# Optimization experiments

Measured on AMD Instinct MI355X. Metric: run time of the kernel, lower is better.

Reference implementation:

```python
import jax, jax.numpy as jnp
import numpy as np

# ---- para constants (see shape_source) ----
SIZE = 200          # SLM / detector plane
PAD = 100           # para.paddings -> padded FFT plane 400x400
PADDED = SIZE + 2 * PAD
NUM_LAYERS = 4
SCALE = 2.0         # para.scale
EXT = 1.0           # para.extension
K = 8               # para.kernel_size
S = 8               # para.stride
M = (SIZE - K) // S + 1   # para.map_size = 25
WIN = 5             # para.win_size
T = 1.0             # softmax temperature
RANGE = 10          # para.range (== dim_out)
DIM_OUT = 10
HIDDEN = 512
DIM_IN = M * M      # 625, flattened BN output feeds fcl
THR = 0.2           # para.thershold
SHIFT = 0.0         # para.shift
EPS = 1e-5          # BatchNorm eps
BATCH = 32


def setup_inputs() -> dict:
    key = jax.random.key(0)
    ks = jax.random.split(key, 10)
    x = jax.random.uniform(ks[0], (BATCH, SIZE, SIZE), jnp.float32)

    def transfer(k):  # unit-magnitude angular-spectrum transfer function
        ph = jax.random.uniform(k, (PADDED, PADDED), jnp.float32, 0.0, 2.0 * np.pi)
        return jnp.exp(1j * ph).astype(jnp.complex64)

    h = transfer(ks[1])
    h_pro = transfer(ks[2])
    h_det = transfer(ks[3])
    phase = 0.1 * jax.random.normal(ks[4], (NUM_LAYERS, SIZE, SIZE), jnp.float32)
    W1 = 0.02 * jax.random.normal(ks[5], (HIDDEN, DIM_IN), jnp.float32)
    b1 = jnp.zeros((HIDDEN,), jnp.float32)
    W2 = 0.02 * jax.random.normal(ks[6], (DIM_OUT, HIDDEN), jnp.float32)
    b2 = jnp.zeros((DIM_OUT,), jnp.float32)
    gamma = jnp.ones((1,), jnp.float32)   # BatchNorm2d(1) weight
    beta = jnp.zeros((1,), jnp.float32)   # BatchNorm2d(1) bias
    return {"x": x, "batch_size": BATCH, "h": h, "h_pro": h_pro, "h_det": h_det,
            "phase": phase, "W1": W1, "b1": b1, "W2": W2, "b2": b2,
            "gamma": gamma, "beta": beta}


def _diff(wave, trans):
    # F.pad + fftshift/fft2 * trans / ifft2/ifftshift (batch-dim shifts cancel)
    wave = jnp.pad(wave, ((0, 0), (PAD, PAD), (PAD, PAD)))
    wf = jnp.fft.fft2(jnp.fft.fftshift(wave, axes=(-2, -1)))
    return jnp.fft.ifftshift(jnp.fft.ifft2(wf * trans), axes=(-2, -1))


def _forward(x, batch_size, h, h_pro, h_det, phase, W1, b1, W2, b2, gamma, beta):
    x = x.astype(jnp.complex64)
    x = _diff(x, h_pro)[:, PAD:PAD + SIZE, PAD:PAD + SIZE]
    for idx in range(NUM_LAYERS):
        trans = jnp.pad(phase[idx], ((PAD, PAD), (PAD, PAD)))
        w = _diff(x, h)
        w = w * jnp.exp(1j * SCALE * jnp.pi * (jnp.sin(EXT * trans) + 1.0))
        x = w[:, PAD:PAD + SIZE, PAD:PAD + SIZE]
    x = _diff(x, h_det)[:, PAD:PAD + SIZE, PAD:PAD + SIZE]
    i_out = jnp.square(jnp.abs(x))                       # (B, SIZE, SIZE)
    B = i_out.shape[0]
    # AvgPool2d(K, S) with SIZE % K == 0 -> reshape-mean
    pooled = i_out.reshape(B, M, K, M, K).mean(axis=(2, 4))  # (B, M, M)

    rows = jnp.arange(M)

    def window(i, j):
        rm = (rows >= i) & (rows < i + WIN)
        cm = (rows >= j) & (rows < j + WIN)
        mask = (rm[:, None] & cm[None, :]).astype(pooled.dtype)   # I_block
        sig = pooled * mask                                       # (B, M, M)
        # BatchNorm2d(1), training mode: stats over all N*H*W
        mu = sig.mean()
        var = sig.var()
        nrm = (sig - mu) / jnp.sqrt(var + EPS) * gamma[0] + beta[0]
        f = nrm.reshape(B, -1)                                    # (B, DIM_IN)
        hid = jax.nn.relu(f @ W1.T + b1)                          # dropout: eval
        logits = (hid @ W2.T + b2) / T
        p = jax.nn.softmax(logits, axis=1)                        # (B, DIM_OUT)
        a = jnp.argmax(p, axis=1)                                 # (B,)
        delta = p.max(axis=1) - p.min(axis=1)                     # b - b2
        temp = jax.nn.one_hot(a, RANGE + 1, dtype=jnp.float32).sum(0)
        final0 = jnp.argmax(temp)
        dm = delta * (a == final0).astype(delta.dtype)            # delta * delta_max
        nz = jnp.sum(dm != 0.0)                                   # csr .data length
        delta1 = jnp.where(nz > 0, dm.sum() / jnp.maximum(nz, 1).astype(dm.dtype), jnp.nan)
        # nan < THR is False, matching torch semantics
        final = jnp.where(delta1 < THR, 0, final0 + 1).astype(jnp.int32)
        res = jnp.where(final == 0, 0.0, final.astype(jnp.float32) + SHIFT)
        ch = (final != 0).astype(jnp.float32)
        return final, res, ch

    ii, jj = jnp.meshgrid(jnp.arange(M), jnp.arange(M), indexing="ij")
    finals, result, ch_map = jax.vmap(window)(ii.ravel(), jj.ravel())
    result = result.reshape(M, M)
    ch_map = ch_map.reshape(M, M)
    histo = jnp.zeros(RANGE + 1, jnp.float32).at[finals].add(1.0)
    return result, ch_map, histo


def reference(x, batch_size, h, h_pro, h_det, phase, W1, b1, W2, b2, gamma, beta):
    return _forward(x, batch_size, h, h_pro, h_det, phase, W1, b1, W2, b2, gamma, beta)
```

## Files before the change

kernel.cpp:

```cpp
#include <hip/hip_runtime.h>
#include <math.h>

#define GLIM_X    1280000
#define GLIM_H    160000
#define GLIM_PH   160000
#define GLIM_W1   320000
#define GLIM_B1   512
#define GLIM_W2   5120
#define GLIM_B2   10
#define GLIM_OUT  1261
#define GLIM_POOL 20000

#define HPART 128

struct cplx { float x, y; };
__device__ __forceinline__ cplx operator+(cplx a, cplx b){ return {a.x+b.x, a.y+b.y}; }
__device__ __forceinline__ cplx operator-(cplx a, cplx b){ return {a.x-b.x, a.y-b.y}; }
__device__ __forceinline__ cplx cmul(cplx a, cplx b){ return {a.x*b.x - a.y*b.y, a.x*b.y + a.y*b.x}; }
template<bool INV>
__device__ __forceinline__ cplx tw(cplx a, cplx w){
  if(INV) return {a.x*w.x + a.y*w.y, a.y*w.x - a.x*w.y};
  else    return {a.x*w.x - a.y*w.y, a.x*w.y + a.y*w.x};
}
template<bool INV>
__device__ __forceinline__ void dft4(cplx&a, cplx&b, cplx&c, cplx&d){
  cplx t0=a+c, t1=a-c, t2=b+d, t3=b-d;
  cplx j3 = INV ? cplx{-t3.y, t3.x} : cplx{t3.y, -t3.x};
  a = t0+t2; c = t0-t2; b = t1+j3; d = t1-j3;
}
template<bool INV>
__device__ void fft16(cplx* x, const cplx* tab){
  cplx y[16];
  #pragma unroll
  for(int b=0;b<4;b++){
    cplx p0=x[b], p1=x[4+b], p2=x[8+b], p3=x[12+b];
    dft4<INV>(p0,p1,p2,p3);
    y[b*4+0]=p0;
    y[b*4+1]=tw<INV>(p1, tab[25*b]);
    y[b*4+2]=tw<INV>(p2, tab[50*b]);
    y[b*4+3]=tw<INV>(p3, tab[75*b]);
  }
  #pragma unroll
  for(int c=0;c<4;c++){
    cplx p0=y[c], p1=y[4+c], p2=y[8+c], p3=y[12+c];
    dft4<INV>(p0,p1,p2,p3);
    x[c]=p0; x[c+4]=p1; x[c+8]=p2; x[c+12]=p3;
  }
}
template<bool INV>
__device__ __forceinline__ void dft5(const cplx* v, cplx* o, const cplx* tab){
  #pragma unroll
  for(int k=0;k<5;k++){
    cplx s=v[0];
    #pragma unroll
    for(int j=1;j<5;j++){
      const int m=(j*k)%5;
      s = s + tw<INV>(v[j], tab[80*m]);
    }
    o[k]=s;
  }
}
template<bool INV>
__device__ void fft25(cplx* t, const cplx* tab){
  cplx u[25];
  #pragma unroll
  for(int b=0;b<5;b++){
    cplx v[5], o[5];
    #pragma unroll
    for(int a=0;a<5;a++) v[a]=t[5*a+b];
    dft5<INV>(v,o,tab);
    #pragma unroll
    for(int c=0;c<5;c++) u[b*5+c]=tw<INV>(o[c], tab[16*b*c]);
  }
  #pragma unroll
  for(int c=0;c<5;c++){
    cplx v[5], o[5];
    #pragma unroll
    for(int b=0;b<5;b++) v[b]=u[b*5+c];
    dft5<INV>(v,o,tab);
    #pragma unroll
    for(int d=0;d<5;d++) t[c+5*d]=o[d];
  }
}

__device__ __forceinline__ float bf2f(unsigned short u){
  unsigned int v = ((unsigned int)u)<<16;
  float f; __builtin_memcpy(&f,&v,4); return f;
}
__device__ __forceinline__ float hf2f(unsigned short u){
  _Float16 x; __builtin_memcpy(&x,&u,2); return (float)x;
}
__device__ __forceinline__ cplx ldH(const void* p, int i, int dec){
  if(i<0 || i>=GLIM_H) return {0.f,0.f};
  unsigned int v = ((const unsigned int*)p)[i];
  unsigned short lo=(unsigned short)(v&0xFFFFu), hi=(unsigned short)(v>>16);
  cplx z;
  if(dec==2)      z = { hf2f(lo), hf2f(hi) };
  else if(dec==3) z = { (float)(short)lo*(1.f/32767.f), (float)(short)hi*(1.f/32767.f) };
  else            z = { bf2f(lo), bf2f(hi) };
  if(!(fabsf(z.x) < 2.f)) z.x = 0.f;
  if(!(fabsf(z.y) < 2.f)) z.y = 0.f;
  return z;
}
__device__ __forceinline__ float ldf(const float* p, int i, int lim){
  if(i<0 || i>=lim) return 0.f;
  return p[i];
}
__device__ __forceinline__ void stout(float* p, int i, float v){
  if(i>=0 && i<GLIM_OUT) p[i] = v;
}

__global__ __launch_bounds__(64) void k_probe(const void* h, int* flags){
  __shared__ float err[3];
  if(threadIdx.x<3) err[threadIdx.x]=0.f;
  __syncthreads();
  if(threadIdx.x<32){
    unsigned int v = ((const unsigned int*)h)[threadIdx.x];
    unsigned short lo=(unsigned short)(v&0xFFFFu), hi=(unsigned short)(v>>16);
    float cr[3], ci[3];
    cr[0]=bf2f(lo);                       ci[0]=bf2f(hi);
    cr[1]=hf2f(lo);                       ci[1]=hf2f(hi);
    cr[2]=(float)(short)lo*(1.f/32767.f); ci[2]=(float)(short)hi*(1.f/32767.f);
    for(int d=0;d<3;d++){
      float r2 = cr[d]*cr[d] + ci[d]*ci[d];
      float e = fabsf(r2 - 1.f);
      if(!(e < 4.f)) e = 4.f;
      atomicAdd(&err[d], e);
    }
  }
  __syncthreads();
  if(threadIdx.x==0){
    int best=0; float be=err[0];
    for(int d=1; d<3; d++) if(err[d] < be){ be=err[d]; best=d; }
    flags[1] = best+1;
    flags[0] = 0;
  }
}

__global__ __launch_bounds__(256) void k_init(cplx* tab, float* outz, float* hist, float* pr){
  int t = blockIdx.x*256 + threadIdx.x;
  if(t < 400){
    float a = -6.28318530717958647692f * (float)t * (1.0f/400.0f);
    float sn, cs; sincosf(a, &sn, &cs);
    tab[t] = { cs, sn };
  }
  if(t < GLIM_OUT) outz[t] = 0.f;
  if(t < 11) hist[t] = 0.f;
  if(t >= 16 && t < 30) pr[t-16] = 0.f;
}

__global__ __launch_bounds__(256) void k_hprep(const void* h, const void* hpro,
    const void* hdet, cplx* __restrict__ Hd, const int* __restrict__ flags)
{
  int dec = flags[1];
  int t = blockIdx.x*256 + threadIdx.x;
  if(t >= 3*GLIM_H) return;
  int arr = t/GLIM_H, o = t - arr*GLIM_H;
  int c = o/400, rem = o - c*400;
  int k1 = rem/25, k2 = rem - k1*25;
  const void* src = (arr==0)?h:((arr==1)?hpro:hdet);
  Hd[t] = ldH(src, (k1+16*k2)*400 + c, dec);
}

__global__ __launch_bounds__(256,2) void k_rowfft(const float* __restrict__ xr,
    int img0, cplx* __restrict__ A, const cplx* __restrict__ gtab, int alim, int nimg)
{
  __shared__ cplx lt[8*400];
  __shared__ cplx stab[400];
  for(int m=threadIdx.x;m<400;m+=256) stab[m]=gtab[m];
  int lr = threadIdx.x>>5, role = threadIdx.x&31;
  int img_local = blockIdx.x % nimg;
  int rc = (blockIdx.x / nimg)*8 + lr;
  int abase = img_local*80000 + rc*400;
  __syncthreads();
  if(role<25){
    int n2=role;
    cplx x[16];
    #pragma unroll
    for(int n1=0;n1<16;n1++){
      cplx v={0.f,0.f};
      if(n1>=4 && n1<12){
        int cc = 25*n1+n2-100;
        v = { ldf(xr, (img0+img_local)*40000 + rc*200 + cc, GLIM_X), 0.f };
      }
      x[n1]=v;
    }
    fft16<false>(x, stab);
    cplx* L = lt + lr*400;
    #pragma unroll
    for(int k1=0;k1<16;k1++) L[k1*25+n2]=tw<false>(x[k1], stab[n2*k1]);
  }
  __syncthreads();
  if(role<16){
    int k1=role;
    cplx* L = lt + lr*400;
    cplx t[25];
    #pragma unroll
    for(int n2=0;n2<25;n2++) t[n2]=L[k1*25+n2];
    fft25<false>(t, stab);
    #pragma unroll
    for(int k2=0;k2<25;k2++){
      int ai = abase + k1+16*k2;
      if(ai>=0 && ai<alim) A[ai]=t[k2];
    }
  }
}

__global__ __launch_bounds__(512,2) void k_colpass(cplx* __restrict__ A,
    const cplx* __restrict__ Hd, const cplx* __restrict__ gtab, int nimg)
{
  __shared__ cplx lt[16*401];
  __shared__ cplx stab[400];
  for(int m=threadIdx.x;m<400;m+=512) stab[m]=gtab[m];
  int img_local = blockIdx.x % nimg, cg = blockIdx.x / nimg;
  int col0 = cg*16;
  int lc = threadIdx.x&15, rr = threadIdx.x>>4;
  int abase = img_local*80000 + col0 + lc;
  cplx* L = lt + lc*401;
  cplx xx[25];
  __syncthreads();
  if(rr<25){
    int n2=rr;
    #pragma unroll
    for(int n1=0;n1<16;n1++){
      cplx v={0.f,0.f};
      if(n1>=4 && n1<12) v = A[abase + (25*n1+n2-100)*400];
      xx[n1]=v;
    }
    fft16<false>(xx, stab);
    #pragma unroll
    for(int k1=0;k1<16;k1++) L[k1*25+n2]=tw<false>(xx[k1], stab[n2*k1]);
  }
  __syncthreads();
  if(rr<16){
    int k1=rr;
    #pragma unroll
    for(int n2=0;n2<25;n2++) xx[n2]=L[k1*25+n2];
    fft25<false>(xx, stab);
    const cplx* hrun = Hd + (col0+lc)*400 + k1*25;
    #pragma unroll
    for(int k2=0;k2<25;k2++) L[k1*25+k2]=cmul(xx[k2], hrun[k2]);
  }
  __syncthreads();
  if(rr<25){
    int n2=rr;
    #pragma unroll
    for(int n1=0;n1<16;n1++){
      int m = 25*n1+n2;
      xx[n1] = L[(m&15)*25 + (m>>4)];
    }
  }
  __syncthreads();
  if(rr<25){
    int n2=rr;
    fft16<true>(xx, stab);
    #pragma unroll
    for(int k1=0;k1<16;k1++) L[k1*25+n2]=tw<true>(xx[k1], stab[n2*k1]);
  }
  __syncthreads();
  if(rr<16){
    int k1=rr;
    #pragma unroll
    for(int n2=0;n2<25;n2++) xx[n2]=L[k1*25+n2];
    fft25<true>(xx, stab);
    const float sc=1.0f/400.0f;
    #pragma unroll
    for(int k2=0;k2<25;k2++){
      int m=k1+16*k2;
      if(m>=100 && m<300) A[abase + (m-100)*400] = { xx[k2].x*sc, xx[k2].y*sc };
    }
  }
}

__global__ __launch_bounds__(512,2) void k_rowpass(cplx* __restrict__ A,
    const float* __restrict__ ph, int phoff, int useMask,
    const cplx* __restrict__ gtab, int alim, int nimg)
{
  __shared__ cplx lt[16*401];
  __shared__ cplx stab[400];
  for(int m=threadIdx.x;m<400;m+=512) stab[m]=gtab[m];
  int lc = threadIdx.x&15, rr = threadIdx.x>>4;
  int img_local = blockIdx.x % nimg, rg = blockIdx.x / nimg;
  int rc = rg*16 + lc;
  int valid = rc < 200;
  int abase = img_local*80000 + rc*400;
  cplx* L = lt + lc*401;
  cplx xx[25];
  __syncthreads();
  if(rr<25){
    int n2=rr;
    #pragma unroll
    for(int n1=0;n1<16;n1++){
      cplx v={0.f,0.f};
      int ai = abase + 25*n1+n2;
      if(valid && ai>=0 && ai<alim) v=A[ai];
      xx[n1]=v;
    }
    fft16<true>(xx, stab);
    #pragma unroll
    for(int k1=0;k1<16;k1++) L[k1*25+n2]=tw<true>(xx[k1], stab[n2*k1]);
  }
  __syncthreads();
  if(rr<16){
    int k1=rr;
    #pragma unroll
    for(int n2=0;n2<25;n2++) xx[n2]=L[k1*25+n2];
    fft25<true>(xx, stab);
    const float sc=1.0f/400.0f;
    #pragma unroll
    for(int k2=0;k2<25;k2++){
      int m=k1+16*k2;
      if(m>=100 && m<300){
        int cc=m-100;
        cplx v={ xx[k2].x*sc, xx[k2].y*sc };
        if(useMask){
          float tt = ldf(ph, phoff + rc*200+cc, GLIM_PH);
          float th = 6.28318530717958647692f*(sinf(tt)+1.0f);
          float sn, cs; sincosf(th,&sn,&cs);
          v = cmul(v, cplx{cs,sn});
        }
        xx[k2]=v;
      }
    }
  }
  __syncthreads();
  if(rr<16){
    int k1=rr;
    #pragma unroll
    for(int k2=0;k2<25;k2++){
      int m=k1+16*k2;
      if(m>=100 && m<300) L[m-100]=xx[k2];
    }
  }
  __syncthreads();
  if(rr<25){
    int n2=rr;
    #pragma unroll
    for(int n1=0;n1<16;n1++){
      cplx v={0.f,0.f};
      if(n1>=4 && n1<12) v = L[25*n1+n2-100];
      xx[n1]=v;
    }
    fft16<false>(xx, stab);
    #pragma unroll
    for(int k1=0;k1<16;k1++) L[k1*25+n2]=tw<false>(xx[k1], stab[n2*k1]);
  }
  __syncthreads();
  if(rr<16){
    int k1=rr;
    #pragma unroll
    for(int n2=0;n2<25;n2++) xx[n2]=L[k1*25+n2];
    fft25<false>(xx, stab);
    if(valid){
      #pragma unroll
      for(int k2=0;k2<25;k2++){
        int ai = abase + k1+16*k2;
        if(ai>=0 && ai<alim) A[ai]=xx[k2];
      }
    }
  }
}

__global__ __launch_bounds__(256,2) void k_rowpool(const cplx* __restrict__ A,
    float* __restrict__ pooled, int img0, const cplx* __restrict__ gtab, int alim, int nimg)
{
  __shared__ cplx lt[8*400];
  __shared__ cplx stab[400];
  __shared__ float sI[8][200];
  for(int m=threadIdx.x;m<400;m+=256) stab[m]=gtab[m];
  int lr=threadIdx.x>>5, role=threadIdx.x&31;
  int img_local = blockIdx.x % nimg, rg = blockIdx.x / nimg;
  int abase = img_local*80000 + (rg*8+lr)*400;
  __syncthreads();
  if(role<25){
    int n2=role;
    cplx x[16];
    #pragma unroll
    for(int n1=0;n1<16;n1++){
      cplx v={0.f,0.f};
      int ai = abase + 25*n1+n2;
      if(ai>=0 && ai<alim) v=A[ai];
      x[n1]=v;
    }
    fft16<true>(x, stab);
    cplx* L = lt + lr*400;
    #pragma unroll
    for(int k1=0;k1<16;k1++) L[k1*25+n2]=tw<true>(x[k1], stab[n2*k1]);
  }
  __syncthreads();
  cplx t[25];
  int k1 = role;
  if(role<16){
    cplx* L=lt+lr*400;
    #pragma unroll
    for(int n2=0;n2<25;n2++) t[n2]=L[k1*25+n2];
    fft25<true>(t, stab);
    const float sc=1.0f/400.0f;
    #pragma unroll
    for(int k2=0;k2<25;k2++){ t[k2].x*=sc; t[k2].y*=sc; }
  }
  if(role<16){
    #pragma unroll
    for(int k2=0;k2<25;k2++){
      int m=k1+16*k2;
      if(m>=100 && m<300) sI[lr][m-100] = t[k2].x*t[k2].x + t[k2].y*t[k2].y;
    }
  }
  __syncthreads();
  if(threadIdx.x<25){
    int il = img_local, r0 = rg*8;
    float s=0.f;
    #pragma unroll
    for(int u=0;u<8;u++){
      #pragma unroll
      for(int v=0;v<8;v++) s += sI[u][threadIdx.x*8+v];
    }
    int pi = (img0+il)*625 + (r0>>3)*25 + threadIdx.x;
    if(pi>=0 && pi<GLIM_POOL) pooled[pi] = s*(1.0f/64.0f);
  }
}

__global__ __launch_bounds__(64) void k_rowsum(const float* __restrict__ W1,
    float* __restrict__ rs){
  __shared__ float red[64];
  int hh = blockIdx.x;
  float s=0.f;
  for(int e=threadIdx.x;e<625;e+=64) s += ldf(W1, hh*625+e, GLIM_W1);
  red[threadIdx.x]=s;
  __syncthreads();
  for(int off=32;off>0;off>>=1){
    if(threadIdx.x<off) red[threadIdx.x]+=red[threadIdx.x+off];
    __syncthreads();
  }
  if(threadIdx.x==0 && hh<512) rs[hh]=red[0];
}

__global__ __launch_bounds__(256,2) void k_window(const float* __restrict__ pooled,
    const float* __restrict__ W1, const float* __restrict__ b1,
    const float* __restrict__ W2, const float* __restrict__ rowsum,
    const float* __restrict__ gm, const float* __restrict__ bt,
    float* __restrict__ LP)
{
  __shared__ float w1s[HPART*26];
  __shared__ float w2s[10*HPART];
  __shared__ float ps[25*32];
  __shared__ float comb[HPART];
  __shared__ int   wIdx[25];
  __shared__ float sred[4][2];
  __shared__ float sf0, sgos;

  int wi = blockIdx.x >> 2;
  int part = blockIdx.x & 3;
  int h0 = part*HPART;
  int i = wi/25, j = wi - i*25;
  int er = (25-i<5)?(25-i):5;
  int ec = (25-j<5)?(25-j):5;
  int E = er*ec;
  int tid = threadIdx.x;
  if(tid<25) wIdx[tid] = (i + tid/ec)*25 + (j + tid%ec);
  __syncthreads();

  for(int t=tid;t<10*HPART;t+=256) w2s[t] = ldf(W2, (t>>7)*512 + h0 + (t&(HPART-1)), GLIM_W2);

  for(int t=tid;t<800;t+=256){
    int e=t>>5;
    float v=0.f;
    if(e<E){
      v = pooled[(t&31)*625 + wIdx[e]];
      if(!(fabsf(v) < 1e30f)) v = 0.f;
    }
    ps[t]=v;
  }

  if(E==25){
    for(int t=tid;t<HPART*25;t+=256){
      int hh=t/25, e=t-hh*25;
      w1s[hh*26+e] = ldf(W1, (h0+hh)*625+wIdx[e], GLIM_W1);
    }
  } else {
    for(int t=tid;t<832;t+=256) ((float4*)w1s)[t] = float4{0.f,0.f,0.f,0.f};
    __syncthreads();
    for(int t=tid;t<HPART*E;t+=256){
      int hh=t/E, e=t-hh*E;
      w1s[hh*26+e] = ldf(W1, (h0+hh)*625+wIdx[e], GLIM_W1);
    }
  }
  __syncthreads();

  {
    float s1=0.f, s2=0.f;
    for(int t=tid;t<800;t+=256){ float v=ps[t]; s1+=v; s2+=v*v; }
    #pragma unroll
    for(int m=1;m<64;m<<=1){ s1 += __shfl_xor(s1,m); s2 += __shfl_xor(s2,m); }
    if((tid&63)==0){ sred[tid>>6][0]=s1; sred[tid>>6][1]=s2; }
  }
  __syncthreads();
  if(tid==0){
    float a=sred[0][0]+sred[1][0]+sred[2][0]+sred[3][0];
    float c=sred[0][1]+sred[1][1]+sred[2][1]+sred[3][1];
    float mu = a*(1.0f/20000.0f);
    float var = c*(1.0f/20000.0f) - mu*mu;
    float sg = sqrtf(var + 1e-5f);
    float g = gm[0];
    sf0 = bt[0] - g*mu/sg;
    sgos = g/sg;
  }
  __syncthreads();
  float f0=sf0, gos=sgos;
  for(int hh=tid;hh<HPART;hh+=256) comb[hh] = ldf(b1,h0+hh,GLIM_B1) + f0*ldf(rowsum,h0+hh,512);
  __syncthreads();

  int b = tid&31, s = tid>>5;
  float psr[25];
  #pragma unroll
  for(int e=0;e<25;e++) psr[e]=ps[e*32+b];

  float pl[10];
  #pragma unroll
  for(int o=0;o<10;o++) pl[o]=0.f;
  for(int k=0;k<16;k++){
    int hh = s*16+k;
    const float* wr = &w1s[hh*26];
    float wsum=0.f;
    #pragma unroll
    for(int e=0;e<25;e++) wsum = fmaf(wr[e], psr[e], wsum);
    float acc = comb[hh] + gos*wsum;
    float hid = acc>0.f?acc:0.f;
    #pragma unroll
    for(int o=0;o<10;o++) pl[o] = fmaf(hid, w2s[o*HPART+hh], pl[o]);
  }
  __syncthreads();
  float* red = w1s;
  #pragma unroll
  for(int o=0;o<10;o++) red[(s*32+b)*10+o]=pl[o];
  __syncthreads();

  if(tid<32){
    #pragma unroll
    for(int o=0;o<10;o++){
      float a = 0.f;
      #pragma unroll
      for(int u=0;u<8;u++) a += red[(u*32+tid)*10+o];
      LP[((part*625+wi)*32+tid)*10+o] = a;
    }
  }
}

__global__ __launch_bounds__(64) void k_vote(const float* __restrict__ LP,
    const float* __restrict__ b2, float* __restrict__ outp, float* __restrict__ hist)
{
  __shared__ int aArr[32];
  __shared__ float dArr[32];
  int wi = blockIdx.x, tid = threadIdx.x;
  if(tid<32){
    float lg[10];
    #pragma unroll
    for(int o=0;o<10;o++){
      float a = ldf(b2,o,GLIM_B2);
      #pragma unroll
      for(int p=0;p<4;p++) a += LP[((p*625+wi)*32+tid)*10+o];
      lg[o]=a;
    }
    float lmax=lg[0]; int am=0;
    #pragma unroll
    for(int o=1;o<10;o++) if(lg[o]>lmax){lmax=lg[o]; am=o;}
    float lmin=lg[0];
    #pragma unroll
    for(int o=1;o<10;o++) lmin=fminf(lmin,lg[o]);
    float Z=0.f;
    #pragma unroll
    for(int o=0;o<10;o++) Z += expf(lg[o]-lmax);
    float delta = (1.f - expf(lmin-lmax))/Z;
    aArr[tid]=am; dArr[tid]=delta;
  }
  __syncthreads();
  if(tid==0){
    int votes[11];
    #pragma unroll
    for(int k=0;k<11;k++) votes[k]=0;
    for(int bb=0;bb<32;bb++){
      int a=aArr[bb];
      if(a>=0 && a<11) votes[a]++;
    }
    int f0i=0, bv=votes[0];
    #pragma unroll
    for(int k=1;k<11;k++) if(votes[k]>bv){bv=votes[k]; f0i=k;}
    float sum=0.f; int nz=0;
    for(int bb=0;bb<32;bb++){
      if(aArr[bb]==f0i){
        float dd=dArr[bb];
        sum+=dd;
        if(dd!=0.f) nz++;
      }
    }
    int fin;
    if(nz>0){
      float d1=sum/(float)nz;
      fin = (d1<0.2f)?0:(f0i+1);
    } else fin = f0i+1;
    stout(outp, wi, (fin==0)?0.f:(float)fin);
    stout(outp, 625+wi, (fin!=0)?1.f:0.f);
    if(fin>=0 && fin<=10) atomicAdd(&hist[fin], 1.0f);
  }
}

__global__ __launch_bounds__(64) void k_fin(const float* __restrict__ hist,
    float* __restrict__ outp){
  if(threadIdx.x<11) stout(outp, 1250+threadIdx.x, hist[threadIdx.x]);
}

__global__ __launch_bounds__(256) void k_diag(const float* __restrict__ pooled,
    const float* __restrict__ hist, const float* __restrict__ pr,
    const int* __restrict__ flags, float* __restrict__ outp){
  __shared__ float smax[256];
  __shared__ int snan[256];
  float m=0.f; int nan=0;
  for(int i=threadIdx.x;i<GLIM_POOL;i+=256){
    float v=pooled[i];
    if(isnan(v)||isinf(v)) nan=1;
    else { float a=fabsf(v); if(a>m)m=a; }
  }
  smax[threadIdx.x]=m; snan[threadIdx.x]=nan;
  __syncthreads();
  for(int off=128;off>0;off>>=1){
    if(threadIdx.x<off){
      smax[threadIdx.x]=fmaxf(smax[threadIdx.x],smax[threadIdx.x+off]);
      snan[threadIdx.x]|=snan[threadIdx.x+off];
    }
    __syncthreads();
  }
  if(threadIdx.x==0 && hist[0] < 613.f){
    int dec = flags[1] & 7;
    int low, nanbit = 0;
    if(snan[0]){ nanbit=128; low=0; (void)pr; }
    else {
      if(smax[0]<=0.f) low=0;
      else {
        int e=(int)floorf(log2f(smax[0]));
        low = e+8; if(low<1)low=1; if(low>15)low=15;
      }
    }
    int S = nanbit | (dec<<4) | low;
    outp[0] = 8192.0f*(float)S;
  }
}

extern "C" void kernel_launch(void* const* d_in, const int* in_sizes, int n_in,
                              void* d_out, int out_size, void* d_ws, size_t ws_size,
                              hipStream_t stream)
{
  (void)in_sizes;
  if(n_in != 12 || out_size < GLIM_OUT || d_ws == nullptr) return;
  const float* x   = (const float*)d_in[0];
  const void* h    = d_in[2];
  const void* hpro = d_in[3];
  const void* hdet = d_in[4];
  const float* phase=(const float*)d_in[5];
  const float* W1  = (const float*)d_in[6];
  const float* b1  = (const float*)d_in[7];
  const float* W2  = (const float*)d_in[8];
  const float* b2  = (const float*)d_in[9];
  const float* gm  = (const float*)d_in[10];
  const float* bt  = (const float*)d_in[11];
  float* out = (float*)d_out;

  const size_t FIXED = 85888ull;
  const size_t HDB   = 3ull*GLIM_H*8ull;
  const size_t ABase = FIXED + HDB;
  int n = 0;
  if     (ABase + 32ull*640000ull <= ws_size) n = 32;
  else if(ABase + 16ull*640000ull <= ws_size) n = 16;
  else if(ABase +  8ull*640000ull <= ws_size) n = 8;
  else if(ABase +  4ull*640000ull <= ws_size) n = 4;
  else if(ABase +  2ull*640000ull <= ws_size) n = 2;
  else if(ABase +  1ull*640000ull <= ws_size) n = 1;
  if(n==0) return;

  char* w = (char*)d_ws;
  int*   flags  = (int*)(w + 0);
  cplx*  tab    = (cplx*)(w + 256);
  float* rowsum = (float*)(w + 3584);
  float* hist   = (float*)(w + 5632);
  float* pr     = (float*)(w + 5760);
  float* pooled = (float*)(w + 5888);
  cplx*  Hd     = (cplx*)(w + FIXED);
  cplx*  A      = (cplx*)(w + ABase);
  float* LP     = (float*)Hd;
  const int alim  = n*80000;

  k_probe<<<1,64,0,stream>>>(h, flags);
  k_init<<<6,256,0,stream>>>(tab, out, hist, pr);
  k_rowsum<<<512,64,0,stream>>>(W1, rowsum);
  k_hprep<<<(3*GLIM_H+255)/256,256,0,stream>>>(h, hpro, hdet, Hd, flags);

  for(int c=0; c<32; c+=n){
    k_rowfft<<<n*25,256,0,stream>>>(x, c, A, tab, alim, n);
    for(int d=0; d<6; d++){
      const cplx* Hcur = (d==0) ? (Hd+GLIM_H) : ((d==5) ? (Hd+2*GLIM_H) : Hd);
      k_colpass<<<n*25,512,0,stream>>>(A, Hcur, tab, n);
      if(d<5){
        int useMask = (d>=1) ? 1 : 0;
        int phoff = useMask ? (d-1)*40000 : 0;
        k_rowpass<<<n*13,512,0,stream>>>(A, phase, phoff, useMask, tab, alim, n);
      } else {
        k_rowpool<<<n*25,256,0,stream>>>(A, pooled, c, tab, alim, n);
      }
    }
  }
  k_window<<<2500,256,0,stream>>>(pooled, W1,b1,W2,rowsum, gm,bt, LP);
  k_vote<<<625,64,0,stream>>>(LP, b2, out, hist);
  k_fin<<<1,64,0,stream>>>(hist, out);
  k_diag<<<1,256,0,stream>>>(pooled, hist, pr, flags, out);
}
```

Measured before the change: 655.0 us.

## Exploit zero-padding in radix-16 FFT stage, raise occupancy, overlap loads with table fill

Adds an fft16zp variant that assumes only the middle 8 of 16 inputs are nonzero. It uses the structure of the zero padding to skip half of the first-stage butterflies, and it is applied to the padded forward FFTs in the rowfft, colpass and rowpass kernels. Global loads are now issued before the shared twiddle table is filled, so their latency overlaps the table copy and the barrier. The launch-bounds waves-per-EU hint is raised from 2 to 4, which may force register limits and cause spills in these heavily unrolled kernels.

```diff
diff --git a/kernel.cpp b/kernel.cpp
--- a/kernel.cpp
+++ b/kernel.cpp
@@ -39,6 +39,29 @@
     y[b*4+1]=tw<INV>(p1, tab[25*b]);
     y[b*4+2]=tw<INV>(p2, tab[50*b]);
     y[b*4+3]=tw<INV>(p3, tab[75*b]);
+  }
+  #pragma unroll
+  for(int c=0;c<4;c++){
+    cplx p0=y[c], p1=y[4+c], p2=y[8+c], p3=y[12+c];
+    dft4<INV>(p0,p1,p2,p3);
+    x[c]=p0; x[c+4]=p1; x[c+8]=p2; x[c+12]=p3;
+  }
+}
+template<bool INV>
+__device__ void fft16zp(cplx* x, const cplx* tab){
+  cplx y[16];
+  #pragma unroll
+  for(int b=0;b<4;b++){
+    cplx p1=x[4+b], p2=x[8+b];
+    cplx j3 = INV ? cplx{-p1.y, p1.x} : cplx{p1.y, -p1.x};
+    cplx a  = p1+p2;
+    cplx bb = { j3.x - p2.x,  j3.y - p2.y };
+    cplx c0 = p2-p1;
+    cplx d  = { -p2.x - j3.x, -p2.y - j3.y };
+    y[b*4+0]=a;
+    y[b*4+1]=tw<INV>(bb, tab[25*b]);
+    y[b*4+2]=tw<INV>(c0, tab[50*b]);
+    y[b*4+3]=tw<INV>(d, tab[75*b]);
   }
   #pragma unroll
   for(int c=0;c<4;c++){
@@ -162,30 +185,29 @@
   Hd[t] = ldH(src, (k1+16*k2)*400 + c, dec);
 }
 
-__global__ __launch_bounds__(256,2) void k_rowfft(const float* __restrict__ xr,
+__global__ __launch_bounds__(256,4) void k_rowfft(const float* __restrict__ xr,
     int img0, cplx* __restrict__ A, const cplx* __restrict__ gtab, int alim, int nimg)
 {
   __shared__ cplx lt[8*400];
   __shared__ cplx stab[400];
-  for(int m=threadIdx.x;m<400;m+=256) stab[m]=gtab[m];
   int lr = threadIdx.x>>5, role = threadIdx.x&31;
   int img_local = blockIdx.x % nimg;
   int rc = (blockIdx.x / nimg)*8 + lr;
   int abase = img_local*80000 + rc*400;
-  __syncthreads();
+  cplx x[16];
   if(role<25){
     int n2=role;
-    cplx x[16];
-    #pragma unroll
-    for(int n1=0;n1<16;n1++){
-      cplx v={0.f,0.f};
-      if(n1>=4 && n1<12){
-        int cc = 25*n1+n2-100;
-        v = { ldf(xr, (img0+img_local)*40000 + rc*200 + cc, GLIM_X), 0.f };
-      }
-      x[n1]=v;
-    }
-    fft16<false>(x, stab);
+    #pragma unroll
+    for(int n1=4;n1<12;n1++){
+      int cc = 25*n1+n2-100;
+      x[n1] = { ldf(xr, (img0+img_local)*40000 + rc*200 + cc, GLIM_X), 0.f };
+    }
+  }
+  for(int m=threadIdx.x;m<400;m+=256) stab[m]=gtab[m];
+  __syncthreads();
+  if(role<25){
+    int n2=role;
+    fft16zp<false>(x, stab);
     cplx* L = lt + lr*400;
     #pragma unroll
     for(int k1=0;k1<16;k1++) L[k1*25+n2]=tw<false>(x[k1], stab[n2*k1]);
@@ -206,28 +228,27 @@
   }
 }
 
-__global__ __launch_bounds__(512,2) void k_colpass(cplx* __restrict__ A,
+__global__ __launch_bounds__(512,4) void k_colpass(cplx* __restrict__ A,
     const cplx* __restrict__ Hd, const cplx* __restrict__ gtab, int nimg)
 {
   __shared__ cplx lt[16*401];
   __shared__ cplx stab[400];
-  for(int m=threadIdx.x;m<400;m+=512) stab[m]=gtab[m];
   int img_local = blockIdx.x % nimg, cg = blockIdx.x / nimg;
   int col0 = cg*16;
   int lc = threadIdx.x&15, rr = threadIdx.x>>4;
   int abase = img_local*80000 + col0 + lc;
   cplx* L = lt + lc*401;
   cplx xx[25];
-  __syncthreads();
   if(rr<25){
     int n2=rr;
     #pragma unroll
-    for(int n1=0;n1<16;n1++){
-      cplx v={0.f,0.f};
-      if(n1>=4 && n1<12) v = A[abase + (25*n1+n2-100)*400];
-      xx[n1]=v;
-    }
-    fft16<false>(xx, stab);
+    for(int n1=4;n1<12;n1++) xx[n1] = A[abase + (25*n1+n2-100)*400];
+  }
+  for(int m=threadIdx.x;m<400;m+=512) stab[m]=gtab[m];
+  __syncthreads();
+  if(rr<25){
+    int n2=rr;
+    fft16zp<false>(xx, stab);
     #pragma unroll
     for(int k1=0;k1<16;k1++) L[k1*25+n2]=tw<false>(xx[k1], stab[n2*k1]);
   }
@@ -272,13 +293,12 @@
   }
 }
 
-__global__ __launch_bounds__(512,2) void k_rowpass(cplx* __restrict__ A,
+__global__ __launch_bounds__(512,4) void k_rowpass(cplx* __restrict__ A,
     const float* __restrict__ ph, int phoff, int useMask,
     const cplx* __restrict__ gtab, int alim, int nimg)
 {
   __shared__ cplx lt[16*401];
   __shared__ cplx stab[400];
-  for(int m=threadIdx.x;m<400;m+=512) stab[m]=gtab[m];
   int lc = threadIdx.x&15, rr = threadIdx.x>>4;
   int img_local = blockIdx.x % nimg, rg = blockIdx.x / nimg;
   int rc = rg*16 + lc;
@@ -286,7 +306,6 @@
   int abase = img_local*80000 + rc*400;
   cplx* L = lt + lc*401;
   cplx xx[25];
-  __syncthreads();
   if(rr<25){
     int n2=rr;
     #pragma unroll
@@ -296,6 +315,11 @@
       if(valid && ai>=0 && ai<alim) v=A[ai];
       xx[n1]=v;
     }
+  }
+  for(int m=threadIdx.x;m<400;m+=512) stab[m]=gtab[m];
+  __syncthreads();
+  if(rr<25){
+    int n2=rr;
     fft16<true>(xx, stab);
     #pragma unroll
     for(int k1=0;k1<16;k1++) L[k1*25+n2]=tw<true>(xx[k1], stab[n2*k1]);
@@ -336,12 +360,8 @@
   if(rr<25){
     int n2=rr;
     #pragma unroll
-    for(int n1=0;n1<16;n1++){
-      cplx v={0.f,0.f};
-      if(n1>=4 && n1<12) v = L[25*n1+n2-100];
-      xx[n1]=v;
-    }
-    fft16<false>(xx, stab);
+    for(int n1=4;n1<12;n1++) xx[n1] = L[25*n1+n2-100];
+    fft16zp<false>(xx, stab);
     #pragma unroll
     for(int k1=0;k1<16;k1++) L[k1*25+n2]=tw<false>(xx[k1], stab[n2*k1]);
   }
@@ -361,7 +381,7 @@
   }
 }
 
-__global__ __launch_bounds__(256,2) void k_rowpool(const cplx* __restrict__ A,
+__global__ __launch_bounds__(256,4) void k_rowpool(const cplx* __restrict__ A,
     float* __restrict__ pooled, int img0, const cplx* __restrict__ gtab, int alim, int nimg)
 {
   __shared__ cplx lt[8*400];
```

Result: slower. 1.474 ms (+125.0%).
